# Kernel tuning notes

Hardware: AMD Instinct MI355X
Metric: run time of the kernel (lower is better)

Reference implementation:

```python
import jax, jax.numpy as jnp
import numpy as np

N, D, K = 500_000, 64, 512


def setup_inputs() -> dict:
    key = jax.random.key(0)
    kx, kc = jax.random.split(key)
    x = jax.random.normal(kx, (N, D), dtype=jnp.float32)
    centroids = jax.random.normal(kc, (K, D), dtype=jnp.float32)
    return {"x": x, "centroids": centroids}


def reference(x, centroids):
    x2 = jnp.sum(x * x, axis=1, keepdims=True)            # [N, 1]
    c2 = jnp.sum(centroids * centroids, axis=1)           # [K]
    d2 = x2 + c2[None, :] - 2.0 * jnp.einsum('nd,kd->nk', x, centroids)
    d2 = jnp.maximum(d2, 0.0)
    # sqrt is monotonic so argmin over d2 == argmin over cdist
    label = jnp.argmin(d2, axis=1)                        # [N] int
    return label
```

## Files before the change

### kernel.cpp

```cpp
#include <hip/hip_runtime.h>

#define DIM 64
#define KC 512
#define BLKM 512
#define BLKP 256
#define PT 4
#define CG 256
#define NT (CG / 16)
#define MARGINH 7.5e-4f
#define LIST_CAP 500000

typedef _Float16 half8   __attribute__((ext_vector_type(8)));
typedef float    floatx4 __attribute__((ext_vector_type(4)));

__device__ __forceinline__ void async_cp16(_Float16* lds_base, const _Float16* g_lane) {
    __builtin_amdgcn_global_load_lds(
        (const __attribute__((address_space(1))) unsigned int*)(g_lane),
        (__attribute__((address_space(3))) unsigned int*)(lds_base),
        16, 0, 0);
}

__global__ __launch_bounds__(BLKP) void kmeans_prep(
    const float* __restrict__ c, _Float16* __restrict__ frH,
    _Float16* __restrict__ frL, float* __restrict__ g_sc2,
    unsigned* __restrict__ rs_count)
{
    const int b = blockIdx.x;
    if (b < 128) {
        const int e  = b * BLKP + threadIdx.x;
        const int cr = e >> 6, d = e & 63;
        const int T  = cr >> 4, ni = cr & 15;
        const int ch = d >> 5, q = (d >> 3) & 3, j = d & 7;
        const int pos = ((T * 2 + ch) * 64 + (q * 16 + ni)) * 8 + j;
        const float f = c[e];
        const _Float16 h = (_Float16)f;
        frH[pos] = h;
        frL[pos] = (_Float16)((f - (float)h) * 2048.0f);
    } else {
        if (b == 128 && threadIdx.x == 0) *rs_count = 0u;
        const int k = (b - 128) * BLKP + threadIdx.x;
        const float* crow = c + (long)k * DIM;
        float s0 = 0.f, s1 = 0.f, s2 = 0.f, s3 = 0.f;
        #pragma unroll
        for (int d = 0; d < DIM; d += 4) {
            s0 = fmaf(crow[d + 0], crow[d + 0], s0);
            s1 = fmaf(crow[d + 1], crow[d + 1], s1);
            s2 = fmaf(crow[d + 2], crow[d + 2], s2);
            s3 = fmaf(crow[d + 3], crow[d + 3], s3);
        }
        g_sc2[k] = (s0 + s1) + (s2 + s3);
    }
}

__global__ __launch_bounds__(BLKM)
__attribute__((amdgpu_waves_per_eu(2)))
void kmeans_mfma(const float* __restrict__ x,
                 const _Float16* __restrict__ frH, const _Float16* __restrict__ frL,
                 const float* __restrict__ g_sc2, int* __restrict__ out,
                 unsigned* __restrict__ rs_count, int* __restrict__ rs_list, int n)
{
    __shared__ _Float16 shH[NT * 2 * 64 * 8];
    __shared__ _Float16 shL[NT * 2 * 64 * 8];
    __shared__ float    s_sc2[KC];

    const int tid  = threadIdx.x;
    const int wave = tid >> 6;
    const int lane = tid & 63;
    const int nidx = lane & 15;
    const int quad = lane >> 4;

    const long jobBase = ((long)blockIdx.x * 8 + wave) * 64;

    half8 ah[PT][2], al[PT][2];
    #pragma unroll
    for (int pt = 0; pt < PT; ++pt) {
        long row = jobBase + pt * 16 + nidx;
        if (row > (long)n - 1) row = (long)n - 1;
        #pragma unroll
        for (int ch = 0; ch < 2; ++ch) {
            const float* xp = x + row * DIM + ch * 32 + quad * 8;
            float4 v0 = *(const float4*)xp;
            float4 v1 = *(const float4*)(xp + 4);
            float fs[8] = {v0.x, v0.y, v0.z, v0.w, v1.x, v1.y, v1.z, v1.w};
            #pragma unroll
            for (int j = 0; j < 8; ++j) {
                _Float16 h = (_Float16)fs[j];
                ah[pt][ch][j] = h;
                al[pt][ch][j] = (_Float16)((fs[j] - (float)h) * 2048.0f);
            }
        }
    }

    float best[PT][4], sec[PT][4];
    int   bidx[PT][4];
    #pragma unroll
    for (int pt = 0; pt < PT; ++pt)
        #pragma unroll
        for (int r = 0; r < 4; ++r) {
            best[pt][r] = -3.402823466e38f;
            sec[pt][r]  = -3.402823466e38f;
            bidx[pt][r] = 0;
        }

    for (int g = 0; g < 2; ++g) {
        if (g) __syncthreads();

        {
            const _Float16* srcH = frH + (long)g * (NT * 2 * 64 * 8);
            const _Float16* srcL = frL + (long)g * (NT * 2 * 64 * 8);
            #pragma unroll
            for (int ii = 0; ii < 4; ++ii) {
                const int chunk = wave * 256 + ii * 64;
                async_cp16(shH + (long)chunk * 8, srcH + (long)(chunk + lane) * 8);
                async_cp16(shL + (long)chunk * 8, srcL + (long)(chunk + lane) * 8);
            }
        }
        if (g == 0) {
            for (int k2 = tid; k2 < KC; k2 += BLKM) s_sc2[k2] = g_sc2[k2];
        }
        __syncthreads();

        #pragma unroll 2
        for (int t = 0; t < NT; ++t) {
            const half8 bh0 = *(const half8*)&shH[((t * 2 + 0) * 64 + lane) * 8];
            const half8 bh1 = *(const half8*)&shH[((t * 2 + 1) * 64 + lane) * 8];
            const half8 bl0 = *(const half8*)&shL[((t * 2 + 0) * 64 + lane) * 8];
            const half8 bl1 = *(const half8*)&shL[((t * 2 + 1) * 64 + lane) * 8];
            const float negh = -0.5f * s_sc2[g * CG + t * 16 + nidx];
            const int   kidx = g * CG + t * 16 + nidx;
            #pragma unroll
            for (int pt = 0; pt < PT; ++pt) {
                floatx4 am = {negh, negh, negh, negh};
                floatx4 ac = {0.f, 0.f, 0.f, 0.f};
                am = __builtin_amdgcn_mfma_f32_16x16x32_f16(ah[pt][0], bh0, am, 0, 0, 0);
                am = __builtin_amdgcn_mfma_f32_16x16x32_f16(ah[pt][1], bh1, am, 0, 0, 0);
                ac = __builtin_amdgcn_mfma_f32_16x16x32_f16(ah[pt][0], bl0, ac, 0, 0, 0);
                ac = __builtin_amdgcn_mfma_f32_16x16x32_f16(ah[pt][1], bl1, ac, 0, 0, 0);
                ac = __builtin_amdgcn_mfma_f32_16x16x32_f16(al[pt][0], bh0, ac, 0, 0, 0);
                ac = __builtin_amdgcn_mfma_f32_16x16x32_f16(al[pt][1], bh1, ac, 0, 0, 0);
                const floatx4 vv = am + ac * 4.8828125e-4f;
                #pragma unroll
                for (int r = 0; r < 4; ++r) {
                    const bool gt = vv[r] > best[pt][r];
                    sec[pt][r]  = fmaxf(sec[pt][r], gt ? best[pt][r] : vv[r]);
                    best[pt][r] = gt ? vv[r] : best[pt][r];
                    bidx[pt][r] = gt ? kidx  : bidx[pt][r];
                }
            }
        }
    }

    #pragma unroll
    for (int off = 1; off < 16; off <<= 1) {
        #pragma unroll
        for (int pt = 0; pt < PT; ++pt)
            #pragma unroll
            for (int r = 0; r < 4; ++r) {
                const float ob = __shfl_xor(best[pt][r], off, 64);
                const int   oi = __shfl_xor(bidx[pt][r], off, 64);
                const float os = __shfl_xor(sec[pt][r],  off, 64);
                const bool take = (ob > best[pt][r]) ||
                                  (ob == best[pt][r] && oi < bidx[pt][r]);
                const float loser = take ? best[pt][r] : ob;
                sec[pt][r]  = fmaxf(fmaxf(sec[pt][r], os), loser);
                best[pt][r] = take ? ob : best[pt][r];
                bidx[pt][r] = take ? oi : bidx[pt][r];
            }
    }

    const int pt_w = nidx >> 2;
    const int r_w  = lane & 3;
    float b = 0.f, s = 0.f; int bi = 0;
    #pragma unroll
    for (int pt = 0; pt < PT; ++pt)
        #pragma unroll
        for (int r = 0; r < 4; ++r) {
            const bool m = (pt == pt_w) && (r == r_w);
            b  = m ? best[pt][r] : b;
            s  = m ? sec[pt][r]  : s;
            bi = m ? bidx[pt][r] : bi;
        }
    const long p = jobBase + (long)pt_w * 16 + quad * 4 + r_w;

    if (p < n) {
        out[p] = bi;
        if (!(b - s > MARGINH)) {
            const unsigned idx = atomicAdd(rs_count, 1u);
            if (idx < LIST_CAP) rs_list[idx] = (int)p;
        }
    }
}

__global__ __launch_bounds__(BLKP) void kmeans_rescan(
    const float* __restrict__ x, const float* __restrict__ c,
    const float* __restrict__ g_sc2, const unsigned* __restrict__ rs_count,
    const int* __restrict__ rs_list, int* __restrict__ out)
{
    const int lane  = threadIdx.x & 63;
    const int gwave = (blockIdx.x * BLKP + threadIdx.x) >> 6;
    const int nwave = gridDim.x * (BLKP / 64);
    unsigned cnt = *rs_count;
    if (cnt > LIST_CAP) cnt = LIST_CAP;

    for (unsigned j = gwave; j < cnt; j += nwave) {
        const int p = rs_list[j];
        const float* xrow = x + (long)p * DIM;

        float x20 = 0.f, x21 = 0.f, x22 = 0.f, x23 = 0.f;
        #pragma unroll
        for (int d = 0; d < DIM; d += 4) {
            x20 = fmaf(xrow[d + 0], xrow[d + 0], x20);
            x21 = fmaf(xrow[d + 1], xrow[d + 1], x21);
            x22 = fmaf(xrow[d + 2], xrow[d + 2], x22);
            x23 = fmaf(xrow[d + 3], xrow[d + 3], x23);
        }
        const float x2 = (x20 + x21) + (x22 + x23);

        float bb = 3.402823466e38f; int bbi = 0x7fffffff;
        #pragma unroll
        for (int kk = 0; kk < 8; ++kk) {
            const int k = lane * 8 + kk;
            const float* crow = c + (long)k * DIM;
            float d0 = 0.f, d1 = 0.f, d2a = 0.f, d3 = 0.f;
            #pragma unroll
            for (int d = 0; d < DIM; d += 4) {
                d0  = fmaf(crow[d + 0], xrow[d + 0], d0);
                d1  = fmaf(crow[d + 1], xrow[d + 1], d1);
                d2a = fmaf(crow[d + 2], xrow[d + 2], d2a);
                d3  = fmaf(crow[d + 3], xrow[d + 3], d3);
            }
            const float dot = (d0 + d1) + (d2a + d3);
            float d2v = (x2 + g_sc2[k]) - 2.0f * dot;
            d2v = fmaxf(d2v, 0.0f);
            const bool l2 = d2v < bb;
            bb  = l2 ? d2v : bb;
            bbi = l2 ? k   : bbi;
        }
        #pragma unroll
        for (int off = 1; off < 64; off <<= 1) {
            const float ob = __shfl_xor(bb, off, 64);
            const int   oi = __shfl_xor(bbi, off, 64);
            const bool take = (ob < bb) || (ob == bb && oi < bbi);
            bb  = take ? ob : bb;
            bbi = take ? oi : bbi;
        }
        if (lane == 0) out[p] = bbi;
    }
}

extern "C" void kernel_launch(void* const* d_in, const int* in_sizes, int n_in,
                              void* d_out, int out_size, void* d_ws, size_t ws_size,
                              hipStream_t stream) {
    const float* x = (const float*)d_in[0];
    const float* c = (const float*)d_in[1];
    int* out = (int*)d_out;
    const int n = in_sizes[0] / DIM;

    _Float16* frH   = (_Float16*)d_ws;
    _Float16* frL   = frH + (KC * DIM);
    float*    gsc2  = (float*)(frL + (KC * DIM));
    unsigned* cnt   = (unsigned*)(gsc2 + KC);
    int*      rlist = (int*)(cnt + 4);

    kmeans_prep<<<130, BLKP, 0, stream>>>(c, frH, frL, gsc2, cnt);

    const int jobs   = (n + 63) / 64;
    const int blocks = (jobs + 7) / 8;
    kmeans_mfma<<<blocks, BLKM, 0, stream>>>(x, frH, frL, gsc2, out, cnt, rlist, n);

    kmeans_rescan<<<128, BLKP, 0, stream>>>(x, c, gsc2, cnt, rlist, out);
}
```

Baseline: 352.8 us.

## Stage all centroids in LDS once, enlarge blocks, tile rescan centroids in LDS

The main kernel now uses 1024-thread blocks of 16 waves and loads all 512 centroid fragments into LDS in one pass. This removes the two-group loop and its extra barrier, and the waves_per_eu hint is dropped. The top-2 tracking uses med3/max in place of compare-and-select. The rescan kernel stages a transposed, padded copy of the centroids and their norms in shared memory with more blocks, instead of reading rows from global memory per lane. The trade-off is more LDS per block in the main kernel, which may lower occupancy, plus a per-block preload cost in the rescan.

```diff
diff --git a/kernel.cpp b/kernel.cpp
--- a/kernel.cpp
+++ b/kernel.cpp
@@ -2,11 +2,12 @@
 
 #define DIM 64
 #define KC 512
-#define BLKM 512
+#define BLKM 1024
+#define WPB 16
 #define BLKP 256
+#define RSB 256
 #define PT 4
-#define CG 256
-#define NT (CG / 16)
+#define NTA 32
 #define MARGINH 7.5e-4f
 #define LIST_CAP 500000
 
@@ -53,14 +54,13 @@
 }
 
 __global__ __launch_bounds__(BLKM)
-__attribute__((amdgpu_waves_per_eu(2)))
 void kmeans_mfma(const float* __restrict__ x,
                  const _Float16* __restrict__ frH, const _Float16* __restrict__ frL,
                  const float* __restrict__ g_sc2, int* __restrict__ out,
                  unsigned* __restrict__ rs_count, int* __restrict__ rs_list, int n)
 {
-    __shared__ _Float16 shH[NT * 2 * 64 * 8];
-    __shared__ _Float16 shL[NT * 2 * 64 * 8];
+    __shared__ _Float16 shH[NTA * 2 * 64 * 8];
+    __shared__ _Float16 shL[NTA * 2 * 64 * 8];
     __shared__ float    s_sc2[KC];
 
     const int tid  = threadIdx.x;
@@ -69,7 +69,15 @@
     const int nidx = lane & 15;
     const int quad = lane >> 4;
 
-    const long jobBase = ((long)blockIdx.x * 8 + wave) * 64;
+    const long jobBase = ((long)blockIdx.x * WPB + wave) * 64;
+
+    #pragma unroll
+    for (int ii = 0; ii < 4; ++ii) {
+        const int chunk = wave * 256 + ii * 64;
+        async_cp16(shH + (long)chunk * 8, frH + (long)(chunk + lane) * 8);
+        async_cp16(shL + (long)chunk * 8, frL + (long)(chunk + lane) * 8);
+    }
+    for (int k2 = tid; k2 < KC; k2 += BLKM) s_sc2[k2] = g_sc2[k2];
 
     half8 ah[PT][2], al[PT][2];
     #pragma unroll
@@ -102,50 +110,33 @@
             bidx[pt][r] = 0;
         }
 
-    for (int g = 0; g < 2; ++g) {
-        if (g) __syncthreads();
-
-        {
-            const _Float16* srcH = frH + (long)g * (NT * 2 * 64 * 8);
-            const _Float16* srcL = frL + (long)g * (NT * 2 * 64 * 8);
-            #pragma unroll
-            for (int ii = 0; ii < 4; ++ii) {
-                const int chunk = wave * 256 + ii * 64;
-                async_cp16(shH + (long)chunk * 8, srcH + (long)(chunk + lane) * 8);
-                async_cp16(shL + (long)chunk * 8, srcL + (long)(chunk + lane) * 8);
-            }
-        }
-        if (g == 0) {
-            for (int k2 = tid; k2 < KC; k2 += BLKM) s_sc2[k2] = g_sc2[k2];
-        }
-        __syncthreads();
-
-        #pragma unroll 2
-        for (int t = 0; t < NT; ++t) {
-            const half8 bh0 = *(const half8*)&shH[((t * 2 + 0) * 64 + lane) * 8];
-            const half8 bh1 = *(const half8*)&shH[((t * 2 + 1) * 64 + lane) * 8];
-            const half8 bl0 = *(const half8*)&shL[((t * 2 + 0) * 64 + lane) * 8];
-            const half8 bl1 = *(const half8*)&shL[((t * 2 + 1) * 64 + lane) * 8];
-            const float negh = -0.5f * s_sc2[g * CG + t * 16 + nidx];
-            const int   kidx = g * CG + t * 16 + nidx;
-            #pragma unroll
-            for (int pt = 0; pt < PT; ++pt) {
-                floatx4 am = {negh, negh, negh, negh};
-                floatx4 ac = {0.f, 0.f, 0.f, 0.f};
-                am = __builtin_amdgcn_mfma_f32_16x16x32_f16(ah[pt][0], bh0, am, 0, 0, 0);
-                am = __builtin_amdgcn_mfma_f32_16x16x32_f16(ah[pt][1], bh1, am, 0, 0, 0);
-                ac = __builtin_amdgcn_mfma_f32_16x16x32_f16(ah[pt][0], bl0, ac, 0, 0, 0);
-                ac = __builtin_amdgcn_mfma_f32_16x16x32_f16(ah[pt][1], bl1, ac, 0, 0, 0);
-                ac = __builtin_amdgcn_mfma_f32_16x16x32_f16(al[pt][0], bh0, ac, 0, 0, 0);
-                ac = __builtin_amdgcn_mfma_f32_16x16x32_f16(al[pt][1], bh1, ac, 0, 0, 0);
-                const floatx4 vv = am + ac * 4.8828125e-4f;
-                #pragma unroll
-                for (int r = 0; r < 4; ++r) {
-                    const bool gt = vv[r] > best[pt][r];
-                    sec[pt][r]  = fmaxf(sec[pt][r], gt ? best[pt][r] : vv[r]);
-                    best[pt][r] = gt ? vv[r] : best[pt][r];
-                    bidx[pt][r] = gt ? kidx  : bidx[pt][r];
-                }
+    __syncthreads();
+
+    #pragma unroll 2
+    for (int t = 0; t < NTA; ++t) {
+        const half8 bh0 = *(const half8*)&shH[((t * 2 + 0) * 64 + lane) * 8];
+        const half8 bh1 = *(const half8*)&shH[((t * 2 + 1) * 64 + lane) * 8];
+        const half8 bl0 = *(const half8*)&shL[((t * 2 + 0) * 64 + lane) * 8];
+        const half8 bl1 = *(const half8*)&shL[((t * 2 + 1) * 64 + lane) * 8];
+        const float negh = -0.5f * s_sc2[t * 16 + nidx];
+        const int   kidx = t * 16 + nidx;
+        #pragma unroll
+        for (int pt = 0; pt < PT; ++pt) {
+            floatx4 am = {negh, negh, negh, negh};
+            floatx4 ac = {0.f, 0.f, 0.f, 0.f};
+            am = __builtin_amdgcn_mfma_f32_16x16x32_f16(ah[pt][0], bh0, am, 0, 0, 0);
+            am = __builtin_amdgcn_mfma_f32_16x16x32_f16(ah[pt][1], bh1, am, 0, 0, 0);
+            ac = __builtin_amdgcn_mfma_f32_16x16x32_f16(ah[pt][0], bl0, ac, 0, 0, 0);
+            ac = __builtin_amdgcn_mfma_f32_16x16x32_f16(ah[pt][1], bl1, ac, 0, 0, 0);
+            ac = __builtin_amdgcn_mfma_f32_16x16x32_f16(al[pt][0], bh0, ac, 0, 0, 0);
+            ac = __builtin_amdgcn_mfma_f32_16x16x32_f16(al[pt][1], bh1, ac, 0, 0, 0);
+            const floatx4 vv = am + ac * 4.8828125e-4f;
+            #pragma unroll
+            for (int r = 0; r < 4; ++r) {
+                const bool gt = vv[r] > best[pt][r];
+                sec[pt][r]  = __builtin_amdgcn_fmed3f(sec[pt][r], vv[r], best[pt][r]);
+                best[pt][r] = fmaxf(best[pt][r], vv[r]);
+                bidx[pt][r] = gt ? kidx : bidx[pt][r];
             }
         }
     }
@@ -191,14 +182,25 @@
     }
 }
 
-__global__ __launch_bounds__(BLKP) void kmeans_rescan(
+__global__ __launch_bounds__(RSB) void kmeans_rescan(
     const float* __restrict__ x, const float* __restrict__ c,
     const float* __restrict__ g_sc2, const unsigned* __restrict__ rs_count,
     const int* __restrict__ rs_list, int* __restrict__ out)
 {
-    const int lane  = threadIdx.x & 63;
-    const int gwave = (blockIdx.x * BLKP + threadIdx.x) >> 6;
-    const int nwave = gridDim.x * (BLKP / 64);
+    __shared__ float4 ct4[16 * 513];
+    __shared__ float  s_c2[KC];
+
+    const int tid = threadIdx.x;
+    for (int e = tid; e < KC * 16; e += RSB) {
+        const int k = e >> 4, d4 = e & 15;
+        ct4[d4 * 513 + k] = *(const float4*)(c + (long)k * DIM + d4 * 4);
+    }
+    for (int k = tid; k < KC; k += RSB) s_c2[k] = g_sc2[k];
+    __syncthreads();
+
+    const int lane  = tid & 63;
+    const int gwave = blockIdx.x * (RSB / 64) + (tid >> 6);
+    const int nwave = gridDim.x * (RSB / 64);
     unsigned cnt = *rs_count;
     if (cnt > LIST_CAP) cnt = LIST_CAP;
 
@@ -219,20 +221,20 @@
         float bb = 3.402823466e38f; int bbi = 0x7fffffff;
         #pragma unroll
         for (int kk = 0; kk < 8; ++kk) {
-            const int k = lane * 8 + kk;
-            const float* crow = c + (long)k * DIM;
+            const int k = kk * 64 + lane;
             float d0 = 0.f, d1 = 0.f, d2a = 0.f, d3 = 0.f;
             #pragma unroll
-            for (int d = 0; d < DIM; d += 4) {
-                d0  = fmaf(crow[d + 0], xrow[d + 0], d0);
-                d1  = fmaf(crow[d + 1], xrow[d + 1], d1);
-                d2a = fmaf(crow[d + 2], xrow[d + 2], d2a);
-                d3  = fmaf(crow[d + 3], xrow[d + 3], d3);
+            for (int d4 = 0; d4 < 16; ++d4) {
+                const float4 q = ct4[d4 * 513 + k];
+                d0  = fmaf(q.x, xrow[4 * d4 + 0], d0);
+                d1  = fmaf(q.y, xrow[4 * d4 + 1], d1);
+                d2a = fmaf(q.z, xrow[4 * d4 + 2], d2a);
+                d3  = fmaf(q.w, xrow[4 * d4 + 3], d3);
             }
             const float dot = (d0 + d1) + (d2a + d3);
-            float d2v = (x2 + g_sc2[k]) - 2.0f * dot;
+            float d2v = (x2 + s_c2[k]) - 2.0f * dot;
             d2v = fmaxf(d2v, 0.0f);
-            const bool l2 = d2v < bb;
+            const bool l2 = (d2v < bb) || (d2v == bb && k < bbi);
             bb  = l2 ? d2v : bb;
             bbi = l2 ? k   : bbi;
         }
@@ -265,8 +267,8 @@
     kmeans_prep<<<130, BLKP, 0, stream>>>(c, frH, frL, gsc2, cnt);
 
     const int jobs   = (n + 63) / 64;
-    const int blocks = (jobs + 7) / 8;
+    const int blocks = (jobs + WPB - 1) / WPB;
     kmeans_mfma<<<blocks, BLKM, 0, stream>>>(x, frH, frL, gsc2, out, cnt, rlist, n);
 
-    kmeans_rescan<<<128, BLKP, 0, stream>>>(x, c, gsc2, cnt, rlist, out);
-}
+    kmeans_rescan<<<256, RSB, 0, stream>>>(x, c, gsc2, cnt, rlist, out);
+}
```

New measurement: 562.8 us. 1.6x slower.
